# Kernel tuning notes

Hardware: AMD Instinct MI355X
Metric: run time of the kernel (lower is better)

Reference implementation:

```python
import jax, jax.numpy as jnp
import numpy as np

N = 100000   # nodes
E = 1600000  # directed edges
D = 128      # feature dim (input = hidden = embedding)
LN_EPS = 1e-5


def setup_inputs() -> dict:
    key = jax.random.key(0)
    ks = jax.random.split(key, 8)
    scale = 1.0 / np.sqrt(D)
    x = jax.random.normal(ks[0], (N, D), dtype=jnp.float32)
    edge_index = jax.random.randint(ks[1], (2, E), 0, N, dtype=jnp.int64)
    W0 = jax.random.normal(ks[2], (D, D), dtype=jnp.float32) * scale
    W1 = jax.random.normal(ks[3], (D, D), dtype=jnp.float32) * scale
    W2 = jax.random.normal(ks[4], (D, D), dtype=jnp.float32) * scale
    b0 = jnp.zeros((D,), jnp.float32)
    b1 = jnp.zeros((D,), jnp.float32)
    b2 = jnp.zeros((D,), jnp.float32)
    ln_g = jnp.ones((D,), jnp.float32)
    ln_b = jnp.zeros((D,), jnp.float32)
    fn_g = jnp.ones((D,), jnp.float32)
    fn_b = jnp.zeros((D,), jnp.float32)
    return {"x": x, "edge_index": edge_index, "W0": W0, "b0": b0,
            "W1": W1, "b1": b1, "W2": W2, "b2": b2,
            "ln_g": ln_g, "ln_b": ln_b, "fn_g": fn_g, "fn_b": fn_b}


def _gcn_conv(x, W, b, src, dst, n):
    # PyG GCNConv: x' = D^{-1/2} (A + I) D^{-1/2} (x W) + b
    h = x @ W                                   # [N, D]
    # add self-loops
    loops = jnp.arange(n, dtype=src.dtype)
    s = jnp.concatenate([src, loops])           # source nodes
    d = jnp.concatenate([dst, loops])           # target nodes
    deg = jax.ops.segment_sum(jnp.ones_like(d, dtype=h.dtype), d, num_segments=n)
    dinv = jnp.where(deg > 0, jax.lax.rsqrt(deg), 0.0)
    norm = dinv[s] * dinv[d]                    # [E+N]
    msg = h[s] * norm[:, None]                  # gather + scale
    out = jax.ops.segment_sum(msg, d, num_segments=n)  # scatter-add at targets
    return out + b


def _layer_norm(x, g, b):
    mu = jnp.mean(x, axis=-1, keepdims=True)
    var = jnp.mean(jnp.square(x - mu), axis=-1, keepdims=True)
    return (x - mu) * jax.lax.rsqrt(var + LN_EPS) * g + b


def reference(x, edge_index, W0, b0, W1, b1, W2, b2, ln_g, ln_b, fn_g, fn_b):
    src, dst = edge_index[0], edge_index[1]
    n = x.shape[0]
    h = jax.nn.relu(_gcn_conv(x, W0, b0, src, dst, n))
    # single middle block (num_gnn_layers=3 -> loop runs for i=1 only)
    identity = h
    h = _layer_norm(h, ln_g, ln_b)
    h = jax.nn.relu(_gcn_conv(h, W1, b1, src, dst, n)) + identity
    h = _gcn_conv(h, W2, b2, src, dst, n)
    return _layer_norm(h, fn_g, fn_b)
```

## Files before the change

### kernel.cpp

```cpp
#include <hip/hip_runtime.h>
#include <hip/hip_bf16.h>

#define DIM 128
#define SB 256
#define NA 256
#define EAMAX 6272
#define BCAP 4096

typedef __attribute__((ext_vector_type(8))) short bf16x8;
typedef __attribute__((ext_vector_type(4))) float f32x4;

__device__ inline float bf2f(unsigned short u) {
    unsigned v = (unsigned)u << 16;
    union { unsigned u; float f; } c; c.u = v; return c.f;
}
__device__ inline unsigned short f2bf(float f) {
    union { __hip_bfloat16 h; unsigned short u; } c;
    c.h = __float2bfloat16(f);
    return c.u;
}


__global__ __launch_bounds__(256) void k_hist(const int* __restrict__ dst,
                                              int* __restrict__ histG,
                                              int E, int EA, int nbuk) {
    __shared__ int h[1024];
    int t = threadIdx.x, blk = blockIdx.x;
    for (int i = t; i < 1024; i += 256) h[i] = 0;
    __syncthreads();
    int lo = blk * EA, hi = min(E, lo + EA);
    for (int i = lo + t; i < hi; i += 256) atomicAdd(&h[dst[i] >> 7], 1);
    __syncthreads();
    for (int bk = t; bk < nbuk; bk += 256) histG[bk * NA + blk] = h[bk];
}

__global__ __launch_bounds__(SB) void k_scan1(const int* __restrict__ cnt,
                                              int* __restrict__ bsum, int n) {
    int t = threadIdx.x;
    int i = blockIdx.x * SB + t;
    int v = (i < n) ? cnt[i] : 0;
#pragma unroll
    for (int m = 1; m < 64; m <<= 1) v += __shfl_xor(v, m);
    __shared__ int w[SB / 64];
    if ((t & 63) == 0) w[t >> 6] = v;
    __syncthreads();
    if (t == 0) {
        int s = 0;
#pragma unroll
        for (int k = 0; k < SB / 64; ++k) s += w[k];
        bsum[blockIdx.x] = s;
    }
}

__global__ __launch_bounds__(1024) void k_scan2(int* __restrict__ bsum, int B) {
    __shared__ int s[1024];
    int t = threadIdx.x;
    int v = (t < B) ? bsum[t] : 0;
    s[t] = v;
    __syncthreads();
    for (int off = 1; off < 1024; off <<= 1) {
        int u = (t >= off) ? s[t - off] : 0;
        __syncthreads();
        s[t] += u;
        __syncthreads();
    }
    if (t < B) bsum[t] = s[t] - v;
}

__global__ __launch_bounds__(SB) void k_scan3g(const int* __restrict__ cnt,
                                               const int* __restrict__ bsum,
                                               int* __restrict__ outx, int n) {
    __shared__ int s[SB];
    int t = threadIdx.x;
    int i = blockIdx.x * SB + t;
    int c = (i < n) ? cnt[i] : 0;
    s[t] = c;
    __syncthreads();
    for (int off = 1; off < SB; off <<= 1) {
        int u = (t >= off) ? s[t - off] : 0;
        __syncthreads();
        s[t] += u;
        __syncthreads();
    }
    int excl = bsum[blockIdx.x] + s[t] - c;
    if (i < n) {
        outx[i] = excl;
        if (i == n - 1) outx[n] = excl + c;
    }
}

__global__ __launch_bounds__(256) void k_place(const int* __restrict__ src,
                                               const int* __restrict__ dst,
                                               const int* __restrict__ scannedG,
                                               unsigned* __restrict__ ebuf,
                                               int E, int EA, int nbuk) {
    __shared__ int h[1024];
    __shared__ int dl[1024];
    __shared__ int ws4[4];
    __shared__ unsigned srt[EAMAX];
    __shared__ unsigned short bkt[EAMAX];
    int t = threadIdx.x, blk = blockIdx.x;
    int lo = blk * EA, hi = min(E, lo + EA);

    for (int i = t; i < 1024; i += 256) h[i] = 0;
    __syncthreads();
    for (int i = lo + t; i < hi; i += 256) atomicAdd(&h[dst[i] >> 7], 1);
    __syncthreads();

    {
        int b4 = t * 4;
        int v0 = h[b4], v1 = h[b4 + 1], v2 = h[b4 + 2], v3 = h[b4 + 3];
        int i1 = v0 + v1, i2 = i1 + v2, i3 = i2 + v3;
        int lane = t & 63, wv = t >> 6;
        int sc = i3;
#pragma unroll
        for (int o = 1; o < 64; o <<= 1) {
            int u = __shfl_up(sc, o);
            if (lane >= o) sc += u;
        }
        if (lane == 63) ws4[wv] = sc;
        __syncthreads();
        int woff = 0;
#pragma unroll
        for (int k = 0; k < 4; ++k) woff += (k < wv) ? ws4[k] : 0;
        int tex = woff + sc - i3;
        h[b4] = tex; h[b4 + 1] = tex + v0; h[b4 + 2] = tex + i1; h[b4 + 3] = tex + i2;
    }
    __syncthreads();

    for (int bk = t; bk < nbuk; bk += 256)
        dl[bk] = scannedG[bk * NA + blk] - h[bk];
    __syncthreads();

    for (int i = lo + t; i < hi; i += 256) {
        int d = dst[i];
        int bk = d >> 7;
        unsigned p = ((unsigned)(d & 127) << 17) | (unsigned)src[i];
        int r = atomicAdd(&h[bk], 1);
        srt[r] = p;
        bkt[r] = (unsigned short)bk;
    }
    __syncthreads();

    int m = hi - lo;
    for (int i = t; i < m; i += 256)
        ebuf[dl[bkt[i]] + i] = srt[i];
}

__global__ __launch_bounds__(256) void k_finish(const unsigned* __restrict__ ebuf,
                                                const int* __restrict__ scannedG,
                                                int* __restrict__ offs,
                                                float* __restrict__ dinv,
                                                int* __restrict__ csrc,
                                                int n, int nbuk) {
    __shared__ unsigned eds[BCAP];
    __shared__ unsigned srt[BCAP];
    __shared__ int lcnt[128], lcur[128];
    __shared__ int wsum[2];
    int b = blockIdx.x, t = threadIdx.x;
    int e0 = scannedG[b * NA], e1 = scannedG[(b + 1) * NA];
    int m = min(e1 - e0, BCAP);

    for (int i = t; i < m; i += 256) eds[i] = ebuf[e0 + i];
    if (t < 128) lcnt[t] = 0;
    __syncthreads();
    for (int i = t; i < m; i += 256) atomicAdd(&lcnt[eds[i] >> 17], 1);
    __syncthreads();

    int c = (t < 128) ? lcnt[t] : 0;
    int lane = t & 63, wv = t >> 6;
    int s = c;
#pragma unroll
    for (int o = 1; o < 64; o <<= 1) {
        int u = __shfl_up(s, o);
        if (lane >= o) s += u;
    }
    if (lane == 63 && wv < 2) wsum[wv] = s;
    __syncthreads();
    int excl = s - c + ((wv == 1) ? wsum[0] : 0);
    if (t < 128) {
        int node = b * 128 + t;
        if (node < n) {
            offs[node] = e0 + excl;
            dinv[node] = rsqrtf((float)(c + 1));
        }
        lcur[t] = excl;
    }
    if (b == nbuk - 1 && t == 0) offs[n] = e1;
    __syncthreads();

    for (int i = t; i < m; i += 256) {
        unsigned v = eds[i];
        int r = atomicAdd(&lcur[v >> 17], 1);
        srt[r] = v & 0x1FFFFu;
    }
    __syncthreads();
    for (int i = t; i < m; i += 256) csrc[e0 + i] = (int)srt[i];
}


__global__ __launch_bounds__(256) void k_gemm(const float* __restrict__ in,
                                              const float* __restrict__ W,
                                              const float* __restrict__ dinv,
                                              unsigned short* __restrict__ outH, int n) {
    __shared__ unsigned short Wt[DIM * 136];
    int t = threadIdx.x;
#pragma unroll
    for (int i = 0; i < 64; ++i) {
        int idx = i * 256 + t;
        int k = idx >> 7, nn = idx & 127;
        Wt[nn * 136 + k] = f2bf(W[idx]);
    }
    __syncthreads();

    int l = t & 63, w = t >> 6;
    int g = l >> 4, li = l & 15;
    int rbase = blockIdx.x * 128 + w * 32;

    f32x4 acc[2][8];
#pragma unroll
    for (int mt = 0; mt < 2; ++mt)
#pragma unroll
        for (int nt = 0; nt < 8; ++nt) acc[mt][nt] = (f32x4)(0.f);

#pragma unroll
    for (int kk = 0; kk < 4; ++kk) {
        bf16x8 a[2];
#pragma unroll
        for (int mt = 0; mt < 2; ++mt) {
            int row = rbase + mt * 16 + li;
            int rr = (row < n) ? row : (n - 1);
            const float* p = in + (size_t)rr * DIM + kk * 32 + g * 8;
            float4 v0 = *(const float4*)p;
            float4 v1 = *(const float4*)(p + 4);
            bf16x8 av;
            av[0] = (short)f2bf(v0.x); av[1] = (short)f2bf(v0.y);
            av[2] = (short)f2bf(v0.z); av[3] = (short)f2bf(v0.w);
            av[4] = (short)f2bf(v1.x); av[5] = (short)f2bf(v1.y);
            av[6] = (short)f2bf(v1.z); av[7] = (short)f2bf(v1.w);
            a[mt] = av;
        }
#pragma unroll
        for (int nt = 0; nt < 8; ++nt) {
            int col = nt * 16 + li;
            bf16x8 bb = *(const bf16x8*)&Wt[col * 136 + kk * 32 + g * 8];
            acc[0][nt] = __builtin_amdgcn_mfma_f32_16x16x32_bf16(a[0], bb, acc[0][nt], 0, 0, 0);
            acc[1][nt] = __builtin_amdgcn_mfma_f32_16x16x32_bf16(a[1], bb, acc[1][nt], 0, 0, 0);
        }
    }

#pragma unroll
    for (int mt = 0; mt < 2; ++mt)
#pragma unroll
        for (int r = 0; r < 4; ++r) {
            int row = rbase + mt * 16 + g * 4 + r;
            if (row < n) {
                float s = dinv[row];
#pragma unroll
                for (int nt = 0; nt < 8; ++nt)
                    outH[(size_t)row * DIM + nt * 16 + li] = f2bf(acc[mt][nt][r] * s);
            }
        }
}


template <int MODE>
__global__ __launch_bounds__(256) void k_agg(const unsigned* __restrict__ H2,
                                             const float* __restrict__ dinv,
                                             const int* __restrict__ offs,
                                             const int* __restrict__ csrc,
                                             const float* __restrict__ bias,
                                             const float* __restrict__ identity,
                                             float* __restrict__ out_raw,
                                             float* __restrict__ out_ln,
                                             const float* __restrict__ lg,
                                             const float* __restrict__ lb, int n) {
    int wv = threadIdx.x >> 6, lane = threadIdx.x & 63;
    int i = blockIdx.x * 4 + wv;
    if (i >= n) return;

    unsigned u0 = H2[(size_t)i * 64 + lane];
    float ax = bf2f((unsigned short)(u0 & 0xffff));
    float ay = bf2f((unsigned short)(u0 >> 16));

    int s = offs[i], e = offs[i + 1];
    int j = s;
    for (; j + 8 <= e; j += 8) {
        unsigned uu[8];
#pragma unroll
        for (int q = 0; q < 8; ++q) uu[q] = H2[(size_t)csrc[j + q] * 64 + lane];
#pragma unroll
        for (int q = 0; q < 8; ++q) {
            ax += bf2f((unsigned short)(uu[q] & 0xffff));
            ay += bf2f((unsigned short)(uu[q] >> 16));
        }
    }
    for (; j < e; ++j) {
        unsigned v = H2[(size_t)csrc[j] * 64 + lane];
        ax += bf2f((unsigned short)(v & 0xffff));
        ay += bf2f((unsigned short)(v >> 16));
    }

    float di = dinv[i];
    float2 bs = ((const float2*)bias)[lane];
    float vx = di * ax + bs.x;
    float vy = di * ay + bs.y;

    float xx, xy;
    if (MODE == 0) { xx = fmaxf(vx, 0.f); xy = fmaxf(vy, 0.f); }
    if (MODE == 1) {
        float2 id = ((const float2*)(identity + (size_t)i * DIM))[lane];
        xx = fmaxf(vx, 0.f) + id.x;
        xy = fmaxf(vy, 0.f) + id.y;
    }
    if (MODE == 2) { xx = vx; xy = vy; }

    if (MODE == 0 || MODE == 1)
        ((float2*)(out_raw + (size_t)i * DIM))[lane] = make_float2(xx, xy);

    if (MODE == 0 || MODE == 2) {
        float su = xx + xy;
#pragma unroll
        for (int m = 1; m < 64; m <<= 1) su += __shfl_xor(su, m);
        float mu = su * (1.f / 128.f);
        float dx = xx - mu, dy = xy - mu;
        float q = dx * dx + dy * dy;
#pragma unroll
        for (int m = 1; m < 64; m <<= 1) q += __shfl_xor(q, m);
        float rstd = rsqrtf(q * (1.f / 128.f) + 1e-5f);
        float2 gg = ((const float2*)lg)[lane];
        float2 bb2 = ((const float2*)lb)[lane];
        ((float2*)(out_ln + (size_t)i * DIM))[lane] =
            make_float2(dx * rstd * gg.x + bb2.x, dy * rstd * gg.y + bb2.y);
    }
}


static inline char* alignp(char* p) {
    return (char*)(((size_t)p + 255) & ~(size_t)255);
}

extern "C" void kernel_launch(void* const* d_in, const int* in_sizes, int n_in,
                              void* d_out, int out_size, void* d_ws, size_t ws_size,
                              hipStream_t stream) {
    const float* x   = (const float*)d_in[0];
    const int*   ei  = (const int*)d_in[1];
    const float* W0  = (const float*)d_in[2];
    const float* b0  = (const float*)d_in[3];
    const float* W1  = (const float*)d_in[4];
    const float* b1  = (const float*)d_in[5];
    const float* W2  = (const float*)d_in[6];
    const float* b2  = (const float*)d_in[7];
    const float* lng = (const float*)d_in[8];
    const float* lnb = (const float*)d_in[9];
    const float* fng = (const float*)d_in[10];
    const float* fnb = (const float*)d_in[11];
    float* out = (float*)d_out;

    int n = in_sizes[0] / DIM;
    int E = in_sizes[1] / 2;
    const int* src = ei;
    const int* dst = ei + E;

    int nbuk = (n + 127) >> 7;
    int EA   = (E + NA - 1) / NA;
    int nh   = nbuk * NA;

    char* p = (char*)d_ws;
    unsigned short* H = (unsigned short*)p;  p = alignp(p + (size_t)n * DIM * 2);
    float* hb   = (float*)p;                 p = alignp(p + (size_t)n * DIM * 4);
    float* dinv = (float*)p;                 p = alignp(p + (size_t)n * 4);
    int*   offs = (int*)p;                   p = alignp(p + (size_t)(n + 1) * 4);
    int*   csrc = (int*)p;                   p = alignp(p + (size_t)E * 4);
    unsigned* ebuf = (unsigned*)p;           p = alignp(p + (size_t)E * 4);
    int*   histG = (int*)p;                  p = alignp(p + (size_t)nh * 4);
    int*   scannedG = (int*)p;               p = alignp(p + (size_t)(nh + 1) * 4);
    int*   bsum = (int*)p;

    int grid_g = (n + 127) / 128;
    int Bs = (nh + SB - 1) / SB;

    k_hist<<<NA, 256, 0, stream>>>(dst, histG, E, EA, nbuk);
    k_scan1<<<Bs, SB, 0, stream>>>(histG, bsum, nh);
    k_scan2<<<1, 1024, 0, stream>>>(bsum, Bs);
    k_scan3g<<<Bs, SB, 0, stream>>>(histG, bsum, scannedG, nh);
    k_place<<<NA, 256, 0, stream>>>(src, dst, scannedG, ebuf, E, EA, nbuk);
    k_finish<<<nbuk, 256, 0, stream>>>(ebuf, scannedG, offs, dinv, csrc, n, nbuk);

    const unsigned* H2 = (const unsigned*)H;
    int grid_a = (n + 3) / 4;

    k_gemm<<<grid_g, 256, 0, stream>>>(x, W0, dinv, H, n);
    k_agg<0><<<grid_a, 256, 0, stream>>>(H2, dinv, offs, csrc, b0, nullptr, hb, out, lng, lnb, n);

    k_gemm<<<grid_g, 256, 0, stream>>>(out, W1, dinv, H, n);
    k_agg<1><<<grid_a, 256, 0, stream>>>(H2, dinv, offs, csrc, b1, hb, hb, nullptr, nullptr, nullptr, n);

    k_gemm<<<grid_g, 256, 0, stream>>>(hb, W2, dinv, H, n);
    k_agg<2><<<grid_a, 256, 0, stream>>>(H2, dinv, offs, csrc, b2, nullptr, nullptr, out, fng, fnb, n);
}
```

Baseline: 370.3 us.

## Store H in feature-sliced layout and aggregate per slice for cache locality

The GEMM output H is written as 8 column slices of 16 features each ([slice][node][16]), and aggregation runs one block per slice per 32 nodes, with 8 lanes per node reading 32 bytes. Each slice (~3.2MB bf16) can then stay resident in L2/LLC while random neighbour gathers hit it, which targets the cache-miss cost of gathering full 256-byte rows across the whole 25MB H. Because one block no longer sees a full row, LayerNorm is split into a separate k_ln kernel. This adds an extra read and write pass over the activations and repeats the CSR index reads once per slice.

```diff
diff --git a/kernel.cpp b/kernel.cpp
--- a/kernel.cpp
+++ b/kernel.cpp
@@ -242,8 +242,7 @@
         }
 #pragma unroll
         for (int nt = 0; nt < 8; ++nt) {
-            int col = nt * 16 + li;
-            bf16x8 bb = *(const bf16x8*)&Wt[col * 136 + kk * 32 + g * 8];
+            bf16x8 bb = *(const bf16x8*)&Wt[(nt * 16 + li) * 136 + kk * 32 + g * 8];
             acc[0][nt] = __builtin_amdgcn_mfma_f32_16x16x32_bf16(a[0], bb, acc[0][nt], 0, 0, 0);
             acc[1][nt] = __builtin_amdgcn_mfma_f32_16x16x32_bf16(a[1], bb, acc[1][nt], 0, 0, 0);
         }
@@ -258,81 +257,94 @@
                 float s = dinv[row];
 #pragma unroll
                 for (int nt = 0; nt < 8; ++nt)
-                    outH[(size_t)row * DIM + nt * 16 + li] = f2bf(acc[mt][nt][r] * s);
+                    outH[((size_t)nt * n + row) * 16 + li] = f2bf(acc[mt][nt][r] * s);
             }
         }
 }
 
 
 template <int MODE>
-__global__ __launch_bounds__(256) void k_agg(const unsigned* __restrict__ H2,
-                                             const float* __restrict__ dinv,
-                                             const int* __restrict__ offs,
-                                             const int* __restrict__ csrc,
-                                             const float* __restrict__ bias,
-                                             const float* __restrict__ identity,
-                                             float* __restrict__ out_raw,
-                                             float* __restrict__ out_ln,
-                                             const float* __restrict__ lg,
-                                             const float* __restrict__ lb, int n) {
+__global__ __launch_bounds__(256) void k_aggs(const unsigned* __restrict__ Hs,
+                                              const float* __restrict__ dinv,
+                                              const int* __restrict__ offs,
+                                              const int* __restrict__ csrc,
+                                              const float* __restrict__ bias,
+                                              const float* __restrict__ identity,
+                                              float* __restrict__ out_raw, int n) {
+    int sl = blockIdx.x & 7;
+    int chunk = blockIdx.x >> 3;
     int wv = threadIdx.x >> 6, lane = threadIdx.x & 63;
-    int i = blockIdx.x * 4 + wv;
-    if (i >= n) return;
-
-    unsigned u0 = H2[(size_t)i * 64 + lane];
+    int slot = lane >> 3, c = lane & 7;
+    int i = chunk * 32 + wv * 8 + slot;
+    bool act = i < n;
+    int ii = act ? i : 0;
+
+    const unsigned* base = Hs + (size_t)sl * n * 8;
+
+    unsigned u0 = base[(size_t)ii * 8 + c];
     float ax = bf2f((unsigned short)(u0 & 0xffff));
     float ay = bf2f((unsigned short)(u0 >> 16));
 
-    int s = offs[i], e = offs[i + 1];
-    int j = s;
-    for (; j + 8 <= e; j += 8) {
-        unsigned uu[8];
-#pragma unroll
-        for (int q = 0; q < 8; ++q) uu[q] = H2[(size_t)csrc[j + q] * 64 + lane];
-#pragma unroll
-        for (int q = 0; q < 8; ++q) {
-            ax += bf2f((unsigned short)(uu[q] & 0xffff));
-            ay += bf2f((unsigned short)(uu[q] >> 16));
-        }
-    }
-    for (; j < e; ++j) {
-        unsigned v = H2[(size_t)csrc[j] * 64 + lane];
+    int s0 = offs[ii], e0 = offs[ii + 1];
+    if (!act) { s0 = 0; e0 = 0; }
+    int j = s0;
+    for (; j + 4 <= e0; j += 4) {
+        int i0 = csrc[j], i1 = csrc[j + 1], i2 = csrc[j + 2], i3 = csrc[j + 3];
+        unsigned v0 = base[(size_t)i0 * 8 + c];
+        unsigned v1 = base[(size_t)i1 * 8 + c];
+        unsigned v2 = base[(size_t)i2 * 8 + c];
+        unsigned v3 = base[(size_t)i3 * 8 + c];
+        ax += bf2f((unsigned short)(v0 & 0xffff)); ay += bf2f((unsigned short)(v0 >> 16));
+        ax += bf2f((unsigned short)(v1 & 0xffff)); ay += bf2f((unsigned short)(v1 >> 16));
+        ax += bf2f((unsigned short)(v2 & 0xffff)); ay += bf2f((unsigned short)(v2 >> 16));
+        ax += bf2f((unsigned short)(v3 & 0xffff)); ay += bf2f((unsigned short)(v3 >> 16));
+    }
+    for (; j < e0; ++j) {
+        unsigned v = base[(size_t)csrc[j] * 8 + c];
         ax += bf2f((unsigned short)(v & 0xffff));
         ay += bf2f((unsigned short)(v >> 16));
     }
 
-    float di = dinv[i];
-    float2 bs = ((const float2*)bias)[lane];
+    int d = sl * 16 + 2 * c;
+    float di = dinv[ii];
+    float2 bs = *(const float2*)(bias + d);
     float vx = di * ax + bs.x;
     float vy = di * ay + bs.y;
 
     float xx, xy;
     if (MODE == 0) { xx = fmaxf(vx, 0.f); xy = fmaxf(vy, 0.f); }
     if (MODE == 1) {
-        float2 id = ((const float2*)(identity + (size_t)i * DIM))[lane];
+        float2 id = *(const float2*)(identity + (size_t)ii * DIM + d);
         xx = fmaxf(vx, 0.f) + id.x;
         xy = fmaxf(vy, 0.f) + id.y;
     }
     if (MODE == 2) { xx = vx; xy = vy; }
 
-    if (MODE == 0 || MODE == 1)
-        ((float2*)(out_raw + (size_t)i * DIM))[lane] = make_float2(xx, xy);
-
-    if (MODE == 0 || MODE == 2) {
-        float su = xx + xy;
-#pragma unroll
-        for (int m = 1; m < 64; m <<= 1) su += __shfl_xor(su, m);
-        float mu = su * (1.f / 128.f);
-        float dx = xx - mu, dy = xy - mu;
-        float q = dx * dx + dy * dy;
-#pragma unroll
-        for (int m = 1; m < 64; m <<= 1) q += __shfl_xor(q, m);
-        float rstd = rsqrtf(q * (1.f / 128.f) + 1e-5f);
-        float2 gg = ((const float2*)lg)[lane];
-        float2 bb2 = ((const float2*)lb)[lane];
-        ((float2*)(out_ln + (size_t)i * DIM))[lane] =
-            make_float2(dx * rstd * gg.x + bb2.x, dy * rstd * gg.y + bb2.y);
-    }
+    if (act) *(float2*)(out_raw + (size_t)i * DIM + d) = make_float2(xx, xy);
+}
+
+
+__global__ __launch_bounds__(256) void k_ln(const float* __restrict__ in,
+                                            const float* __restrict__ g,
+                                            const float* __restrict__ b,
+                                            float* __restrict__ out, int n) {
+    int w = threadIdx.x >> 6, lane = threadIdx.x & 63;
+    int row = blockIdx.x * 4 + w;
+    if (row >= n) return;
+    float2 v = ((const float2*)(in + (size_t)row * DIM))[lane];
+    float s = v.x + v.y;
+#pragma unroll
+    for (int m = 1; m < 64; m <<= 1) s += __shfl_xor(s, m);
+    float mu = s * (1.f / 128.f);
+    float dx = v.x - mu, dy = v.y - mu;
+    float q = dx * dx + dy * dy;
+#pragma unroll
+    for (int m = 1; m < 64; m <<= 1) q += __shfl_xor(q, m);
+    float rstd = rsqrtf(q * (1.f / 128.f) + 1e-5f);
+    float2 gg = ((const float2*)g)[lane];
+    float2 bb = ((const float2*)b)[lane];
+    ((float2*)(out + (size_t)row * DIM))[lane] =
+        make_float2(dx * rstd * gg.x + bb.x, dy * rstd * gg.y + bb.y);
 }
 
 
@@ -388,14 +400,17 @@
     k_finish<<<nbuk, 256, 0, stream>>>(ebuf, scannedG, offs, dinv, csrc, n, nbuk);
 
     const unsigned* H2 = (const unsigned*)H;
-    int grid_a = (n + 3) / 4;
+    int grid_a = ((n + 31) / 32) * 8;
+    int grid_l = (n + 3) / 4;
 
     k_gemm<<<grid_g, 256, 0, stream>>>(x, W0, dinv, H, n);
-    k_agg<0><<<grid_a, 256, 0, stream>>>(H2, dinv, offs, csrc, b0, nullptr, hb, out, lng, lnb, n);
-
+    k_aggs<0><<<grid_a, 256, 0, stream>>>(H2, dinv, offs, csrc, b0, nullptr, hb, n);
+
+    k_ln<<<grid_l, 256, 0, stream>>>(hb, lng, lnb, out, n);
     k_gemm<<<grid_g, 256, 0, stream>>>(out, W1, dinv, H, n);
-    k_agg<1><<<grid_a, 256, 0, stream>>>(H2, dinv, offs, csrc, b1, hb, hb, nullptr, nullptr, nullptr, n);
+    k_aggs<1><<<grid_a, 256, 0, stream>>>(H2, dinv, offs, csrc, b1, hb, hb, n);
 
     k_gemm<<<grid_g, 256, 0, stream>>>(hb, W2, dinv, H, n);
-    k_agg<2><<<grid_a, 256, 0, stream>>>(H2, dinv, offs, csrc, b2, nullptr, nullptr, out, fng, fnb, n);
-}
+    k_aggs<2><<<grid_a, 256, 0, stream>>>(H2, dinv, offs, csrc, b2, nullptr, out, n);
+    k_ln<<<grid_l, 256, 0, stream>>>(out, fng, fnb, out, n);
+}
```

Measured after the change: 460.4 us. +24.3%, slower.
